# Kernel tuning notes

Hardware: AMD Instinct MI355X
Metric: run time of the kernel (lower is better)

Reference implementation:

```python
import jax, jax.numpy as jnp
import numpy as np

B, S, D = 16, 2048, 128

def setup_inputs() -> dict:
    key = jax.random.key(0)
    kq, kk, kv, km = jax.random.split(key, 4)
    Q = jax.random.normal(kq, (B, S, D), dtype=jnp.float32)
    K = jax.random.normal(kk, (B, S, D), dtype=jnp.float32)
    V = jax.random.normal(kv, (B, S, D), dtype=jnp.float32)
    # mask: True entries are masked out (filled with -inf), same as torch.masked_fill_
    mask = jax.random.randint(km, (B, S, S), 0, 2).astype(bool)
    return {"Q": Q, "K": K, "V": V, "mask": mask, "dk": 128}

def reference(Q, K, V, mask, dk):
    # scores: [B, S_q, S_k]
    w = jnp.einsum('bqd,bkd->bqk', Q, K)
    w = jnp.where(mask, -jnp.inf, w)
    # scale applied to masked scores (as in original: mask first, then divide);
    # -inf / scale stays -inf, so math matches exactly.
    scale = jnp.asarray(dk, w.dtype) ** 0.5
    p = jax.nn.softmax(w / scale, axis=-1)
    # context: [B, S_q, D]
    return jnp.einsum('bqk,bkd->bqd', p, V)
```

## Files before the change

### kernel.cpp

```cpp
#include <hip/hip_runtime.h>
#include <hip/hip_bf16.h>
#include <stdint.h>

typedef __attribute__((ext_vector_type(8)))  short short8;
typedef __attribute__((ext_vector_type(4)))  float floatx4;
typedef __attribute__((ext_vector_type(16))) float floatx16;

#define S_LEN 2048
#define DH    128
#define BQ    64
#define BKV   64
#define NSTEP (S_LEN / BKV)
#define SCALE 0.08838834764831845f
#define SCALE2 0.12753785429791905f
#define DTHR 11.541560327111708f

__device__ __forceinline__ float ex2(float x) { return __builtin_amdgcn_exp2f(x); }

__device__ __forceinline__ unsigned short f2b(float f) {
    union { float f; unsigned u; } v; v.f = f;
    unsigned r = v.u + 0x7fffu + ((v.u >> 16) & 1u);
    return (unsigned short)(r >> 16);
}

__device__ __forceinline__ unsigned cvt_pk(float lo, float hi) {
    unsigned r;
    asm("v_cvt_pk_bf16_f32 %0, %1, %2" : "=v"(r) : "v"(lo), "v"(hi));
    return r;
}


__global__ __launch_bounds__(256) void kfrag_make(const float* __restrict__ K,
                                                  unsigned short* __restrict__ KF)
{
    const int T = blockIdx.x, b = blockIdx.y;
    const float* Kb = K + ((size_t)b * S_LEN + T * 64) * DH;
    unsigned short* out = KF + ((size_t)(b * 32 + T)) * 1024 * 8;
    #pragma unroll
    for (int i = 0; i < 4; ++i) {
        int F = i * 256 + threadIdx.x;
        int lq = F & 31, h = (F >> 5) & 1, dsub = (F >> 6) & 7, wk = F >> 9;
        const float* src = Kb + (size_t)(wk * 32 + lq) * DH + dsub * 16 + h * 8;
        float4 a = *(const float4*)src, bb = *(const float4*)(src + 4);
        short8 f;
        f[0] = f2b(a.x);  f[1] = f2b(a.y);  f[2] = f2b(a.z);  f[3] = f2b(a.w);
        f[4] = f2b(bb.x); f[5] = f2b(bb.y); f[6] = f2b(bb.z); f[7] = f2b(bb.w);
        *(short8*)(out + (size_t)F * 8) = f;
    }
}

__global__ __launch_bounds__(256) void vfrag_make(const float* __restrict__ V,
                                                  unsigned short* __restrict__ VF)
{
    __shared__ float t[32][33];
    const int k0 = blockIdx.x * 32, d0 = blockIdx.y * 32, b = blockIdx.z;
    const int tx = threadIdx.x & 31, ty = threadIdx.x >> 5;
    const float* Vb = V + ((size_t)b * S_LEN + k0) * DH + d0;
    #pragma unroll
    for (int i = 0; i < 4; ++i)
        t[ty + 8 * i][tx] = Vb[(size_t)(ty + 8 * i) * DH + tx];
    __syncthreads();
    if (threadIdx.x < 128) {
        const int lq = threadIdx.x & 31;
        const int h  = (threadIdx.x >> 5) & 1;
        const int ks = threadIdx.x >> 6;
        const int T = k0 >> 6, wk = (k0 >> 5) & 1, ds = d0 >> 5;
        short8 f;
        #pragma unroll
        for (int e = 0; e < 8; ++e)
            f[e] = f2b(t[ks * 16 + h * 8 + e][lq]);
        unsigned short* o = VF +
            ((((((size_t)(b * 32 + T) * 4 + ds) * 2 + wk) * 2 + ks) * 2 + h) * 32 + lq) * 8;
        *(short8*)o = f;
    }
}

#define PM_OFF 34816
#define LDS_BYTES 45056

__global__ __launch_bounds__(256, 2)
void attn_fwd(const float* __restrict__ Q, const unsigned short* __restrict__ KF,
              const unsigned short* __restrict__ VF,
              const int* __restrict__ M,
              float* __restrict__ O)
{
    __shared__ __align__(128) char lds[LDS_BYTES];

    const int tid  = threadIdx.x;
    const int lane = tid & 63;
    const int w    = tid >> 6;
    const int wq   = w & 1;
    const int wk   = w >> 1;
    const int lq   = lane & 31;
    const int hi   = lane >> 5;
    const int qt   = blockIdx.x;
    const int b    = blockIdx.y;
    const int q0   = qt * BQ;

    short8 qf[8];
    {
        const float* qrow = Q + ((size_t)(b * S_LEN + q0 + wq * 32 + lq)) * DH;
        #pragma unroll
        for (int dsub = 0; dsub < 8; ++dsub) {
            const float* p = qrow + dsub * 16 + hi * 8;
            float4 a  = *(const float4*)(p);
            float4 bb = *(const float4*)(p + 4);
            short8 f;
            f[0] = f2b(a.x * SCALE2);  f[1] = f2b(a.y * SCALE2);
            f[2] = f2b(a.z * SCALE2);  f[3] = f2b(a.w * SCALE2);
            f[4] = f2b(bb.x * SCALE2); f[5] = f2b(bb.y * SCALE2);
            f[6] = f2b(bb.z * SCALE2); f[7] = f2b(bb.w * SCALE2);
            qf[dsub] = f;
        }
    }

    float m_run = -1e30f;
    float l_run = 0.f;
    floatx16 accO[4];
    #pragma unroll
    for (int i = 0; i < 4; ++i) accO[i] = (floatx16)(0.f);

    const unsigned short* KFl = KF + (((size_t)(b * 32) * 2 + wk) * 512
                                      + (size_t)hi * 32 + lq) * 8;
    const unsigned short* VFl = VF + ((((size_t)(b * 32) * 4 * 2 + wk) * 2) * 2 * 32
                                      + (size_t)hi * 32 + lq) * 8;

    const int* Mq = M + (size_t)b * S_LEN * S_LEN + (size_t)q0 * S_LEN;

    int4 mA[4], mB[4];
    short8 kfc[8], vfc[8];
    unsigned long long mgc[4];

#define LOAD_KF(T) {                                                          \
    const unsigned short* kp_ = KFl + (size_t)(T) * (2 * 512 * 8);            \
    _Pragma("unroll")                                                         \
    for (int dsub = 0; dsub < 8; ++dsub)                                      \
        kfc[dsub] = *(const short8*)(kp_ + dsub * 512);                       \
}

#define LOAD_VF(T) {                                                          \
    _Pragma("unroll")                                                         \
    for (int ds = 0; ds < 4; ++ds)                                            \
        _Pragma("unroll")                                                     \
        for (int ks = 0; ks < 2; ++ks)                                        \
            vfc[ds * 2 + ks] = *(const short8*)(VFl                           \
                + ((size_t)(T) * 16 + ds * 4 + ks) * (2 * 32 * 8));           \
}

#define LOAD_MROWS(DST, G, SB) {                                              \
    _Pragma("unroll")                                                         \
    for (int rr = 0; rr < 4; ++rr)                                            \
        DST[rr] = *(const int4*)(Mq + (size_t)(w * 16 + (SB) * 4 + rr) * S_LEN \
                                 + (G) * 256 + 4 * lane);                     \
}
#define PACK_MROWS(SRC, PBUF, SB) {                                           \
    char* pms_ = lds + PM_OFF + (PBUF) * 2560;                                \
    _Pragma("unroll")                                                         \
    for (int rr = 0; rr < 4; ++rr) {                                          \
        int4 mm = SRC[rr];                                                    \
        unsigned long long b0 = __ballot(mm.x != 0);                          \
        unsigned long long b1 = __ballot(mm.y != 0);                          \
        unsigned long long b2 = __ballot(mm.z != 0);                          \
        unsigned long long b3 = __ballot(mm.w != 0);                          \
        if (lane == 0) {                                                      \
            char* rp_ = pms_ + (w * 16 + (SB) * 4 + rr) * 40;                 \
            *(unsigned long long*)(rp_ +  0) = b0;                            \
            *(unsigned long long*)(rp_ +  8) = b1;                            \
            *(unsigned long long*)(rp_ + 16) = b2;                            \
            *(unsigned long long*)(rp_ + 24) = b3;                            \
        }                                                                     \
    }                                                                         \
}

    #pragma unroll
    for (int gg = 0; gg < 2; ++gg)
        #pragma unroll
        for (int sb = 0; sb < 4; ++sb) {
            int4 t_[4];
            LOAD_MROWS(t_, gg, sb)
            PACK_MROWS(t_, gg, sb)
        }
    __syncthreads();

#define STEP_BODY(T, TT, MCUR, MOLD) {                                        \
    LOAD_KF(T);                                                               \
    LOAD_VF(T);                                                               \
               \
    if ((T) < 24) LOAD_MROWS(MCUR, ((T) >> 2) + 2, TT)                        \
                                     \
    if ((T) >= 1 && (T) <= 24) {                                              \
        const int ps_   = ((T) - 1) & 3;                                      \
        const int pbuf_ = (((((T) - 1) >> 2) + 2) & 3);                       \
        PACK_MROWS(MOLD, pbuf_, ps_)                                          \
    }                                                                         \
                   \
    if ((TT) == 0) {                                                          \
        const char* pmb_ = lds + PM_OFF + (((T) >> 2) & 3) * 2560             \
                           + (wq * 32 + lq) * 40;                             \
        mgc[0] = *(const unsigned long long*)(pmb_ + 0);                      \
        mgc[1] = *(const unsigned long long*)(pmb_ + 8);                      \
        mgc[2] = *(const unsigned long long*)(pmb_ + 16);                     \
        mgc[3] = *(const unsigned long long*)(pmb_ + 24);                     \
    }                                                                         \
                                                                    \
    floatx16 accS = (floatx16)(0.f);                                          \
    __builtin_amdgcn_s_setprio(1);                                            \
    _Pragma("unroll")                                                         \
    for (int dsub = 0; dsub < 8; ++dsub)                                      \
        accS = __builtin_amdgcn_mfma_f32_32x32x16_bf16(                       \
                   kfc[dsub], qf[dsub], accS, 0, 0, 0);                       \
    __builtin_amdgcn_s_setprio(0);                                            \
                    \
    const int base_ = (TT) * 16 + wk * 8 + hi;                                \
    unsigned mb0 = (unsigned)(mgc[0] >> base_);                               \
    unsigned mb1 = (unsigned)(mgc[1] >> base_);                               \
    unsigned mb2 = (unsigned)(mgc[2] >> base_);                               \
    unsigned mb3 = (unsigned)(mgc[3] >> base_);                               \
    float p_[16];                                                             \
    _Pragma("unroll")                                                         \
    for (int j = 0; j < 4; ++j) {                                             \
        p_[4*j+0] = ((mb0 >> (2*j)) & 1u) ? -1e30f : accS[4*j+0];             \
        p_[4*j+1] = ((mb1 >> (2*j)) & 1u) ? -1e30f : accS[4*j+1];             \
        p_[4*j+2] = ((mb2 >> (2*j)) & 1u) ? -1e30f : accS[4*j+2];             \
        p_[4*j+3] = ((mb3 >> (2*j)) & 1u) ? -1e30f : accS[4*j+3];             \
    }                                                                         \
    float mx = p_[0];                                                         \
    _Pragma("unroll")                                                         \
    for (int r = 1; r < 16; ++r) mx = fmaxf(mx, p_[r]);                       \
    mx = fmaxf(mx, __shfl_xor(mx, 32));                                       \
    int need = __any(mx - m_run > DTHR);                                      \
    float corr = 1.0f;                                                        \
    if (need) {                                                               \
        float mn = fmaxf(m_run, mx);                                          \
        corr = ex2(m_run - mn);                                               \
        m_run = mn;                                                           \
    }                                                                         \
    float ts = 0.f;                                                           \
    _Pragma("unroll")                                                         \
    for (int r = 0; r < 16; ++r) { p_[r] = ex2(p_[r] - m_run); ts += p_[r]; } \
    ts += __shfl_xor(ts, 32);                                                 \
    if (need) {                                                               \
        l_run = l_run * corr + ts;                                            \
        _Pragma("unroll")                                                     \
        for (int ds = 0; ds < 4; ++ds) {                                      \
            floatx16 o = accO[ds];                                            \
            _Pragma("unroll")                                                 \
            for (int r = 0; r < 16; ++r) o[r] *= corr;                        \
            accO[ds] = o;                                                     \
        }                                                                     \
    } else {                                                                  \
        l_run += ts;                                                          \
    }                                                                         \
                                 \
    short8 pf[2];                                                             \
    _Pragma("unroll")                                                         \
    for (int ks = 0; ks < 2; ++ks) {                                          \
        unsigned a01 = cvt_pk(p_[8*ks+0], p_[8*ks+1]);                        \
        unsigned a23 = cvt_pk(p_[8*ks+2], p_[8*ks+3]);                        \
        unsigned b01 = cvt_pk(p_[8*ks+4], p_[8*ks+5]);                        \
        unsigned b23 = cvt_pk(p_[8*ks+6], p_[8*ks+7]);                        \
        unsigned ta01 = (unsigned)__shfl_xor((int)a01, 32);                   \
        unsigned ta23 = (unsigned)__shfl_xor((int)a23, 32);                   \
        unsigned tb01 = (unsigned)__shfl_xor((int)b01, 32);                   \
        unsigned tb23 = (unsigned)__shfl_xor((int)b23, 32);                   \
        union { unsigned u[4]; short8 v; } pu;                                \
        pu.u[0] = hi ? tb01 : a01;                                            \
        pu.u[1] = hi ? tb23 : a23;                                            \
        pu.u[2] = hi ? b01 : ta01;                                            \
        pu.u[3] = hi ? b23 : ta23;                                            \
        pf[ks] = pu.v;                                                        \
    }                                                                         \
                                                                      \
    __builtin_amdgcn_s_setprio(1);                                            \
    _Pragma("unroll")                                                         \
    for (int ds = 0; ds < 4; ++ds)                                            \
        _Pragma("unroll")                                                     \
        for (int ks = 0; ks < 2; ++ks)                                        \
            accO[ds] = __builtin_amdgcn_mfma_f32_32x32x16_bf16(               \
                           vfc[ds * 2 + ks], pf[ks], accO[ds], 0, 0, 0);      \
    __builtin_amdgcn_s_setprio(0);                                            \
            \
    if ((TT) == 3) {                                                          \
        asm volatile("s_waitcnt lgkmcnt(0)" ::: "memory");                    \
        __builtin_amdgcn_s_barrier();                                         \
    }                                                                         \
}

    for (int g = 0; g < 8; ++g) {
        STEP_BODY(4 * g + 0, 0, mA, mB)
        STEP_BODY(4 * g + 1, 1, mB, mA)
        STEP_BODY(4 * g + 2, 2, mA, mB)
        STEP_BODY(4 * g + 3, 3, mB, mA)
    }
#undef STEP_BODY
#undef LOAD_KF
#undef LOAD_VF
#undef LOAD_MROWS
#undef PACK_MROWS

    {
        float* mg = (float*)lds;
        const int slot = (wq * 64 + lane) * 68;
        if (wk == 1) {
            #pragma unroll
            for (int ds = 0; ds < 4; ++ds)
                #pragma unroll
                for (int rr = 0; rr < 4; ++rr) {
                    float4 v;
                    v.x = accO[ds][4*rr+0]; v.y = accO[ds][4*rr+1];
                    v.z = accO[ds][4*rr+2]; v.w = accO[ds][4*rr+3];
                    *(float4*)(mg + slot + ds * 16 + rr * 4) = v;
                }
            mg[slot + 64] = m_run;
            mg[slot + 65] = l_run;
        }
        __syncthreads();
        if (wk == 0) {
            float m1 = mg[slot + 64], l1 = mg[slot + 65];
            float m  = fmaxf(m_run, m1);
            float f0 = ex2(m_run - m), f1 = ex2(m1 - m);
            float l  = l_run * f0 + l1 * f1;
            float inv = (l > 0.f) ? 1.f / l : 0.f;
            float* Ob = O + ((size_t)(b * S_LEN + q0 + wq * 32 + lq)) * DH;
            #pragma unroll
            for (int ds = 0; ds < 4; ++ds)
                #pragma unroll
                for (int rr = 0; rr < 4; ++rr) {
                    float4 part = *(const float4*)(mg + slot + ds * 16 + rr * 4);
                    float4 ov;
                    ov.x = (accO[ds][4*rr+0] * f0 + part.x * f1) * inv;
                    ov.y = (accO[ds][4*rr+1] * f0 + part.y * f1) * inv;
                    ov.z = (accO[ds][4*rr+2] * f0 + part.z * f1) * inv;
                    ov.w = (accO[ds][4*rr+3] * f0 + part.w * f1) * inv;
                    *(float4*)(Ob + ds * 32 + 8 * rr + 4 * hi) = ov;
                }
        }
    }
}

#define FB_LDS_BYTES 77824

__global__ __launch_bounds__(256, 2)
void attn_fwd_fb(const float* __restrict__ Q, const float* __restrict__ K,
                 const float* __restrict__ V, const int* __restrict__ M,
                 float* __restrict__ O)
{
    __shared__ __align__(128) char lds[FB_LDS_BYTES];

    const int tid  = threadIdx.x;
    const int lane = tid & 63;
    const int w    = tid >> 6;
    const int c    = lane & 15;
    const int g    = lane >> 4;
    const int qt   = blockIdx.x;
    const int b    = blockIdx.y;
    const int q0   = qt * 64;

    const int rbase = tid >> 5;
    const int c4    = tid & 31;
    const unsigned swk = (unsigned)(c4 * 8) ^ (unsigned)(rbase << 4);
    const int vd    = tid & 127;
    const int vk0   = (tid >> 7) * 32;

    short8 qf[4];
    {
        const float* qrow = Q + ((size_t)(b * S_LEN + q0 + w * 16 + c)) * DH;
        #pragma unroll
        for (int dk = 0; dk < 4; ++dk) {
            const float* p = qrow + dk * 32 + g * 8;
            float4 a  = *(const float4*)(p);
            float4 bb = *(const float4*)(p + 4);
            short8 f;
            f[0] = f2b(a.x * SCALE);  f[1] = f2b(a.y * SCALE);
            f[2] = f2b(a.z * SCALE);  f[3] = f2b(a.w * SCALE);
            f[4] = f2b(bb.x * SCALE); f[5] = f2b(bb.y * SCALE);
            f[6] = f2b(bb.z * SCALE); f[7] = f2b(bb.w * SCALE);
            qf[dk] = f;
        }
    }

    float m_run[4] = {-1e30f, -1e30f, -1e30f, -1e30f};
    float l_run[4] = {0.f, 0.f, 0.f, 0.f};
    floatx4 accO[8];
    #pragma unroll
    for (int i = 0; i < 8; ++i) accO[i] = (floatx4)(0.f);

    const float* Kb = K + (size_t)b * S_LEN * DH;
    const float* Vb = V + (size_t)b * S_LEN * DH;
    const int*   Mb = M + (size_t)b * S_LEN * S_LEN + (size_t)q0 * S_LEN;

    size_t moff[4];
    #pragma unroll
    for (int r = 0; r < 4; ++r)
        moff[r] = (size_t)(w * 16 + 4 * g + r) * S_LEN;

    float4 kreg[8];
    float  vreg[32];
    int    mreg[16];

    #pragma unroll
    for (int i = 0; i < 8; ++i)
        kreg[i] = *(const float4*)(Kb + (size_t)(i * 8 + rbase) * DH + c4 * 4);
    #pragma unroll
    for (int j = 0; j < 32; ++j)
        vreg[j] = Vb[(size_t)(vk0 + j) * DH + vd];
    #pragma unroll
    for (int r = 0; r < 4; ++r)
        #pragma unroll
        for (int n = 0; n < 4; ++n)
            mreg[r * 4 + n] = Mb[moff[r] + n * 16 + c];

    #pragma unroll
    for (int i = 0; i < 8; ++i) {
        float4 kv = kreg[i];
        unsigned long long kp =
              (unsigned long long)f2b(kv.x)
            | ((unsigned long long)f2b(kv.y) << 16)
            | ((unsigned long long)f2b(kv.z) << 32)
            | ((unsigned long long)f2b(kv.w) << 48);
        *(unsigned long long*)(lds + (i * 8 + rbase) * 256 + swk) = kp;
    }
    {
        char* vbase = lds + 32768 + vd * 144 + vk0 * 2;
        #pragma unroll
        for (int i = 0; i < 4; ++i) {
            short8 pk;
            #pragma unroll
            for (int e = 0; e < 8; ++e) pk[e] = f2b(vreg[i * 8 + e]);
            *(short8*)(vbase + i * 16) = pk;
        }
    }
    #pragma unroll
    for (int i = 0; i < 8; ++i)
        kreg[i] = *(const float4*)(Kb + (size_t)(BKV + i * 8 + rbase) * DH + c4 * 4);
    #pragma unroll
    for (int j = 0; j < 32; ++j)
        vreg[j] = Vb[(size_t)(BKV + vk0 + j) * DH + vd];

    __syncthreads();

    char* psw = lds + 69632 + w * 2048;

    for (int step = 0; step < NSTEP; ++step) {
        const int p = step & 1;
        const int kv0 = step * BKV;
        char* KHp = lds + p * 16384;
        char* VTp = lds + 32768 + p * 18432;

        floatx4 accS[4];
        #pragma unroll
        for (int n = 0; n < 4; ++n) accS[n] = (floatx4)(0.f);
        #pragma unroll
        for (int n = 0; n < 4; ++n) {
            const char* krow = KHp + (n * 16 + c) * 256;
            #pragma unroll
            for (int dk = 0; dk < 4; ++dk) {
                unsigned colb = (unsigned)(dk * 64 + g * 16) ^ (unsigned)((c & 7) << 4);
                short8 kf = *(const short8*)(krow + colb);
                accS[n] = __builtin_amdgcn_mfma_f32_16x16x32_bf16(qf[dk], kf, accS[n], 0, 0, 0);
            }
        }

        float pv[4][4];
        float corr[4];
        #pragma unroll
        for (int r = 0; r < 4; ++r) {
            float sv[4];
            #pragma unroll
            for (int n = 0; n < 4; ++n) {
                float s = accS[n][r];
                if (mreg[r * 4 + n]) s = -1e30f;
                sv[n] = s;
            }
            float tm = fmaxf(fmaxf(sv[0], sv[1]), fmaxf(sv[2], sv[3]));
            #pragma unroll
            for (int off = 1; off < 16; off <<= 1)
                tm = fmaxf(tm, __shfl_xor(tm, off, 64));
            float mn = fmaxf(m_run[r], tm);
            corr[r]  = __expf(m_run[r] - mn);
            m_run[r] = mn;
            float ts = 0.f;
            #pragma unroll
            for (int n = 0; n < 4; ++n) { pv[n][r] = __expf(sv[n] - mn); ts += pv[n][r]; }
            #pragma unroll
            for (int off = 1; off < 16; off <<= 1)
                ts += __shfl_xor(ts, off, 64);
            l_run[r] = l_run[r] * corr[r] + ts;
        }
        if (step + 1 < NSTEP) {
            const int kvn = kv0 + BKV;
            #pragma unroll
            for (int r = 0; r < 4; ++r)
                #pragma unroll
                for (int n = 0; n < 4; ++n)
                    mreg[r * 4 + n] = Mb[moff[r] + kvn + n * 16 + c];
        }

        #pragma unroll
        for (int s8 = 0; s8 < 8; ++s8) {
            floatx4 o = accO[s8];
            o[0] *= corr[0]; o[1] *= corr[1]; o[2] *= corr[2]; o[3] *= corr[3];
            accO[s8] = o;
        }

        #pragma unroll
        for (int r = 0; r < 4; ++r) {
            int rl = 4 * g + r;
            #pragma unroll
            for (int n = 0; n < 4; ++n) {
                unsigned colb = (unsigned)((n * 16 + c) * 2) ^ (unsigned)((rl & 7) << 4);
                *(unsigned short*)(psw + rl * 128 + colb) = f2b(pv[n][r]);
            }
        }

        #pragma unroll
        for (int sub = 0; sub < 2; ++sub) {
            unsigned colb = (unsigned)(sub * 64 + g * 16) ^ (unsigned)((c & 7) << 4);
            short8 pf = *(const short8*)(psw + c * 128 + colb);
            #pragma unroll
            for (int s8 = 0; s8 < 8; ++s8) {
                short8 vf = *(const short8*)(VTp + (s8 * 16 + c) * 144 + sub * 64 + g * 16);
                accO[s8] = __builtin_amdgcn_mfma_f32_16x16x32_bf16(pf, vf, accO[s8], 0, 0, 0);
            }
        }

        if (step + 1 < NSTEP) {
            char* KHn = lds + (p ^ 1) * 16384;
            char* VTn = lds + 32768 + (p ^ 1) * 18432;
            #pragma unroll
            for (int i = 0; i < 8; ++i) {
                float4 kv = kreg[i];
                unsigned long long kp =
                      (unsigned long long)f2b(kv.x)
                    | ((unsigned long long)f2b(kv.y) << 16)
                    | ((unsigned long long)f2b(kv.z) << 32)
                    | ((unsigned long long)f2b(kv.w) << 48);
                *(unsigned long long*)(KHn + (i * 8 + rbase) * 256 + swk) = kp;
            }
            char* vbase = VTn + vd * 144 + vk0 * 2;
            #pragma unroll
            for (int i = 0; i < 4; ++i) {
                short8 pk;
                #pragma unroll
                for (int e = 0; e < 8; ++e) pk[e] = f2b(vreg[i * 8 + e]);
                *(short8*)(vbase + i * 16) = pk;
            }
            if (step + 2 < NSTEP) {
                const int kvn2 = kv0 + 2 * BKV;
                #pragma unroll
                for (int i = 0; i < 8; ++i)
                    kreg[i] = *(const float4*)(Kb + (size_t)(kvn2 + i * 8 + rbase) * DH + c4 * 4);
                #pragma unroll
                for (int j = 0; j < 32; ++j)
                    vreg[j] = Vb[(size_t)(kvn2 + vk0 + j) * DH + vd];
            }
        }
        __syncthreads();
    }

    float inv[4];
    #pragma unroll
    for (int r = 0; r < 4; ++r) inv[r] = (l_run[r] > 0.f) ? 1.f / l_run[r] : 0.f;
    float* Ob = O + ((size_t)(b * S_LEN + q0 + w * 16)) * DH;
    #pragma unroll
    for (int s8 = 0; s8 < 8; ++s8) {
        #pragma unroll
        for (int r = 0; r < 4; ++r) {
            Ob[(size_t)(4 * g + r) * DH + s8 * 16 + c] = accO[s8][r] * inv[r];
        }
    }
}

extern "C" void kernel_launch(void* const* d_in, const int* in_sizes, int n_in,
                              void* d_out, int out_size, void* d_ws, size_t ws_size,
                              hipStream_t stream) {
    const float* Q = (const float*)d_in[0];
    const float* K = (const float*)d_in[1];
    const float* V = (const float*)d_in[2];
    const int*   M = (const int*)d_in[3];
    float*       O = (float*)d_out;

    const size_t elems    = (size_t)16 * S_LEN * DH;
    const size_t kv_bytes = elems * sizeof(unsigned short);
    if (ws_size >= 2 * kv_bytes) {
        unsigned short* KFp = (unsigned short*)d_ws;
        unsigned short* VFp = (unsigned short*)d_ws + elems;
        kfrag_make<<<dim3(32, 16), dim3(256), 0, stream>>>(K, KFp);
        vfrag_make<<<dim3(S_LEN / 32, DH / 32, 16), dim3(256), 0, stream>>>(V, VFp);
        attn_fwd<<<dim3(S_LEN / BQ, 16), dim3(256), 0, stream>>>(Q, KFp, VFp, M, O);
    } else {
        attn_fwd_fb<<<dim3(S_LEN / 64, 16), dim3(256), 0, stream>>>(Q, K, V, M, O);
    }
}
```

Measured before the change: 113.3 us.

## Split mask loading into dedicated producer warps with barrier-synchronised handoff

```diff
diff --git a/kernel.cpp b/kernel.cpp
--- a/kernel.cpp
+++ b/kernel.cpp
@@ -78,24 +78,83 @@
 #define PM_OFF 34816
 #define LDS_BYTES 45056
 
-__global__ __launch_bounds__(256, 2)
-void attn_fwd(const float* __restrict__ Q, const unsigned short* __restrict__ KF,
-              const unsigned short* __restrict__ VF,
-              const int* __restrict__ M,
-              float* __restrict__ O)
+#define BARRIER_RAW() do {                                             \
+    asm volatile("s_waitcnt lgkmcnt(0)" ::: "memory");                 \
+    __builtin_amdgcn_s_barrier();                                      \
+    asm volatile("" ::: "memory");                                     \
+} while (0)
+
+__global__ __launch_bounds__(384)
+void attn_pc(const float* __restrict__ Q, const unsigned short* __restrict__ KF,
+             const unsigned short* __restrict__ VF,
+             const int* __restrict__ M,
+             float* __restrict__ O)
 {
     __shared__ __align__(128) char lds[LDS_BYTES];
 
     const int tid  = threadIdx.x;
     const int lane = tid & 63;
     const int w    = tid >> 6;
-    const int wq   = w & 1;
-    const int wk   = w >> 1;
-    const int lq   = lane & 31;
-    const int hi   = lane >> 5;
     const int qt   = blockIdx.x;
     const int b    = blockIdx.y;
     const int q0   = qt * BQ;
+    const int* Mq  = M + (size_t)b * S_LEN * S_LEN + (size_t)q0 * S_LEN;
+
+    if (w >= 4) {
+        const int r0 = (w - 4) * 32;
+        int4 bufA[8], bufB[8];
+
+#define PLOAD(BUF, G, C) {                                                    \
+    _Pragma("unroll")                                                         \
+    for (int rr = 0; rr < 8; ++rr)                                            \
+        BUF[rr] = *(const int4*)(Mq + (size_t)(r0 + (C) * 8 + rr) * S_LEN     \
+                                 + (size_t)(G) * 256 + 4 * lane);             \
+}
+#define PPACK(BUF, G, C) {                                                    \
+    char* pms_ = lds + PM_OFF + ((G) & 3) * 2560;                             \
+    _Pragma("unroll")                                                         \
+    for (int rr = 0; rr < 8; ++rr) {                                          \
+        int4 mm = BUF[rr];                                                    \
+        unsigned long long b0 = __ballot(mm.x != 0);                          \
+        unsigned long long b1 = __ballot(mm.y != 0);                          \
+        unsigned long long b2 = __ballot(mm.z != 0);                          \
+        unsigned long long b3 = __ballot(mm.w != 0);                          \
+        if (lane == 0) {                                                      \
+            char* rp_ = pms_ + (r0 + (C) * 8 + rr) * 40;                      \
+            *(unsigned long long*)(rp_ +  0) = b0;                            \
+            *(unsigned long long*)(rp_ +  8) = b1;                            \
+            *(unsigned long long*)(rp_ + 16) = b2;                            \
+            *(unsigned long long*)(rp_ + 24) = b3;                            \
+        }                                                                     \
+    }                                                                         \
+}
+#define PGROUP(G) {                                                           \
+    PLOAD(bufA, G, 0) PLOAD(bufB, G, 1)                                       \
+    PPACK(bufA, G, 0) PLOAD(bufA, G, 2)                                       \
+    PPACK(bufB, G, 1) PLOAD(bufB, G, 3)                                       \
+    PPACK(bufA, G, 2) PPACK(bufB, G, 3)                                       \
+}
+
+        PGROUP(0)
+        PGROUP(1)
+        BARRIER_RAW();
+        for (int g = 0; g < 6; ++g) {
+            PGROUP(g + 2)
+            BARRIER_RAW();
+        }
+        BARRIER_RAW();
+        BARRIER_RAW();
+        __builtin_amdgcn_s_barrier();
+#undef PGROUP
+#undef PPACK
+#undef PLOAD
+        return;
+    }
+
+    const int wq = w & 1;
+    const int wk = w >> 1;
+    const int lq = lane & 31;
+    const int hi = lane >> 5;
 
     short8 qf[8];
     {
@@ -125,9 +184,6 @@
     const unsigned short* VFl = VF + ((((size_t)(b * 32) * 4 * 2 + wk) * 2) * 2 * 32
                                       + (size_t)hi * 32 + lq) * 8;
 
-    const int* Mq = M + (size_t)b * S_LEN * S_LEN + (size_t)q0 * S_LEN;
-
-    int4 mA[4], mB[4];
     short8 kfc[8], vfc[8];
     unsigned long long mgc[4];
 
@@ -137,7 +193,6 @@
     for (int dsub = 0; dsub < 8; ++dsub)                                      \
         kfc[dsub] = *(const short8*)(kp_ + dsub * 512);                       \
 }
-
 #define LOAD_VF(T) {                                                          \
     _Pragma("unroll")                                                         \
     for (int ds = 0; ds < 4; ++ds)                                            \
@@ -147,53 +202,11 @@
                 + ((size_t)(T) * 16 + ds * 4 + ks) * (2 * 32 * 8));           \
 }
 
-#define LOAD_MROWS(DST, G, SB) {                                              \
-    _Pragma("unroll")                                                         \
-    for (int rr = 0; rr < 4; ++rr)                                            \
-        DST[rr] = *(const int4*)(Mq + (size_t)(w * 16 + (SB) * 4 + rr) * S_LEN \
-                                 + (G) * 256 + 4 * lane);                     \
-}
-#define PACK_MROWS(SRC, PBUF, SB) {                                           \
-    char* pms_ = lds + PM_OFF + (PBUF) * 2560;                                \
-    _Pragma("unroll")                                                         \
-    for (int rr = 0; rr < 4; ++rr) {                                          \
-        int4 mm = SRC[rr];                                                    \
-        unsigned long long b0 = __ballot(mm.x != 0);                          \
-        unsigned long long b1 = __ballot(mm.y != 0);                          \
-        unsigned long long b2 = __ballot(mm.z != 0);                          \
-        unsigned long long b3 = __ballot(mm.w != 0);                          \
-        if (lane == 0) {                                                      \
-            char* rp_ = pms_ + (w * 16 + (SB) * 4 + rr) * 40;                 \
-            *(unsigned long long*)(rp_ +  0) = b0;                            \
-            *(unsigned long long*)(rp_ +  8) = b1;                            \
-            *(unsigned long long*)(rp_ + 16) = b2;                            \
-            *(unsigned long long*)(rp_ + 24) = b3;                            \
-        }                                                                     \
-    }                                                                         \
-}
-
-    #pragma unroll
-    for (int gg = 0; gg < 2; ++gg)
-        #pragma unroll
-        for (int sb = 0; sb < 4; ++sb) {
-            int4 t_[4];
-            LOAD_MROWS(t_, gg, sb)
-            PACK_MROWS(t_, gg, sb)
-        }
-    __syncthreads();
-
-#define STEP_BODY(T, TT, MCUR, MOLD) {                                        \
+    BARRIER_RAW();
+
+#define STEP_BODY(T, TT) {                                                    \
     LOAD_KF(T);                                                               \
     LOAD_VF(T);                                                               \
-               \
-    if ((T) < 24) LOAD_MROWS(MCUR, ((T) >> 2) + 2, TT)                        \
-                                     \
-    if ((T) >= 1 && (T) <= 24) {                                              \
-        const int ps_   = ((T) - 1) & 3;                                      \
-        const int pbuf_ = (((((T) - 1) >> 2) + 2) & 3);                       \
-        PACK_MROWS(MOLD, pbuf_, ps_)                                          \
-    }                                                                         \
-                   \
     if ((TT) == 0) {                                                          \
         const char* pmb_ = lds + PM_OFF + (((T) >> 2) & 3) * 2560             \
                            + (wq * 32 + lq) * 40;                             \
@@ -202,7 +215,6 @@
         mgc[2] = *(const unsigned long long*)(pmb_ + 16);                     \
         mgc[3] = *(const unsigned long long*)(pmb_ + 24);                     \
     }                                                                         \
-                                                                    \
     floatx16 accS = (floatx16)(0.f);                                          \
     __builtin_amdgcn_s_setprio(1);                                            \
     _Pragma("unroll")                                                         \
@@ -210,7 +222,6 @@
         accS = __builtin_amdgcn_mfma_f32_32x32x16_bf16(                       \
                    kfc[dsub], qf[dsub], accS, 0, 0, 0);                       \
     __builtin_amdgcn_s_setprio(0);                                            \
-                    \
     const int base_ = (TT) * 16 + wk * 8 + hi;                                \
     unsigned mb0 = (unsigned)(mgc[0] >> base_);                               \
     unsigned mb1 = (unsigned)(mgc[1] >> base_);                               \
@@ -251,7 +262,6 @@
     } else {                                                                  \
         l_run += ts;                                                          \
     }                                                                         \
-                                 \
     short8 pf[2];                                                             \
     _Pragma("unroll")                                                         \
     for (int ks = 0; ks < 2; ++ks) {                                          \
@@ -270,7 +280,6 @@
         pu.u[3] = hi ? b23 : ta23;                                            \
         pf[ks] = pu.v;                                                        \
     }                                                                         \
-                                                                      \
     __builtin_amdgcn_s_setprio(1);                                            \
     _Pragma("unroll")                                                         \
     for (int ds = 0; ds < 4; ++ds)                                            \
@@ -279,24 +288,18 @@
             accO[ds] = __builtin_amdgcn_mfma_f32_32x32x16_bf16(               \
                            vfc[ds * 2 + ks], pf[ks], accO[ds], 0, 0, 0);      \
     __builtin_amdgcn_s_setprio(0);                                            \
-            \
-    if ((TT) == 3) {                                                          \
-        asm volatile("s_waitcnt lgkmcnt(0)" ::: "memory");                    \
-        __builtin_amdgcn_s_barrier();                                         \
-    }                                                                         \
+    if ((TT) == 3) BARRIER_RAW();                                             \
 }
 
     for (int g = 0; g < 8; ++g) {
-        STEP_BODY(4 * g + 0, 0, mA, mB)
-        STEP_BODY(4 * g + 1, 1, mB, mA)
-        STEP_BODY(4 * g + 2, 2, mA, mB)
-        STEP_BODY(4 * g + 3, 3, mB, mA)
+        STEP_BODY(4 * g + 0, 0)
+        STEP_BODY(4 * g + 1, 1)
+        STEP_BODY(4 * g + 2, 2)
+        STEP_BODY(4 * g + 3, 3)
     }
 #undef STEP_BODY
 #undef LOAD_KF
 #undef LOAD_VF
-#undef LOAD_MROWS
-#undef PACK_MROWS
 
     {
         float* mg = (float*)lds;
@@ -314,7 +317,7 @@
             mg[slot + 64] = m_run;
             mg[slot + 65] = l_run;
         }
-        __syncthreads();
+        BARRIER_RAW();
         if (wk == 0) {
             float m1 = mg[slot + 64], l1 = mg[slot + 65];
             float m  = fmaxf(m_run, m1);
@@ -587,7 +590,7 @@
         unsigned short* VFp = (unsigned short*)d_ws + elems;
         kfrag_make<<<dim3(32, 16), dim3(256), 0, stream>>>(K, KFp);
         vfrag_make<<<dim3(S_LEN / 32, DH / 32, 16), dim3(256), 0, stream>>>(V, VFp);
-        attn_fwd<<<dim3(S_LEN / BQ, 16), dim3(256), 0, stream>>>(Q, KFp, VFp, M, O);
+        attn_pc<<<dim3(S_LEN / BQ, 16), dim3(384), 0, stream>>>(Q, KFp, VFp, M, O);
     } else {
         attn_fwd_fb<<<dim3(S_LEN / 64, 16), dim3(256), 0, stream>>>(Q, K, V, M, O);
     }
```

New measurement: 123.4 us. 8.9% more time.
